# Performance work log

Measured on AMD Instinct MI355X. Metric: run time of the kernel, lower is better.

## Reference

```python
import jax, jax.numpy as jnp
import numpy as np

WD, WH, WW = 2, 7, 7          # window size (D, H, W)
SD, SH, SW = 1, 3, 3          # shift size
DIM, NH = 128, 4              # channels, heads
B, D, H, W = 8, 8, 56, 56     # input dims
N = WD * WH * WW              # tokens per window = 98
HIDDEN = int(DIM * 4.0)


def _rel_index_np():
    coords = np.stack(np.meshgrid(np.arange(WD), np.arange(WH), np.arange(WW), indexing='ij'))
    coords = coords.reshape(3, -1)                      # [3, N]
    rel = (coords[:, :, None] - coords[:, None, :]).transpose(1, 2, 0)  # [N, N, 3]
    rel[:, :, 0] += WD - 1
    rel[:, :, 1] += WH - 1
    rel[:, :, 2] += WW - 1
    rel[:, :, 0] *= (2 * WH - 1) * (2 * WW - 1)
    rel[:, :, 1] *= (2 * WW - 1)
    return rel.sum(-1).astype(np.int32)                 # [N, N]


def _window_partition_np(x):
    b, d, h, w, c = x.shape
    x = x.reshape(b, d // WD, WD, h // WH, WH, w // WW, WW, c)
    return x.transpose(0, 1, 3, 5, 2, 4, 6, 7).reshape(-1, N, c)


def _attn_mask_np():
    img = np.zeros((1, D, H, W, 1), np.float32)
    cnt = 0
    for ds in (slice(0, -WD), slice(-WD, -SD), slice(-SD, None)):
        for hs in (slice(0, -WH), slice(-WH, -SH), slice(-SH, None)):
            for ws in (slice(0, -WW), slice(-WW, -SW), slice(-SW, None)):
                img[:, ds, hs, ws, :] = cnt
                cnt += 1
    mw = _window_partition_np(img).reshape(-1, N)       # [nW, N]
    am = mw[:, None, :] - mw[:, :, None]
    return np.where(am != 0, -100.0, 0.0).astype(np.float32)  # [nW, N, N]


def setup_inputs() -> dict:
    key = jax.random.key(0)
    ks = jax.random.split(key, 8)
    s = 0.02
    return {
        'x': jax.random.normal(ks[0], (B, D, H, W, DIM), jnp.float32),
        'mask_matrix': jnp.asarray(_attn_mask_np()),
        'rel_index': jnp.asarray(_rel_index_np()),
        'norm1_g': jnp.ones((DIM,), jnp.float32),
        'norm1_b': jnp.zeros((DIM,), jnp.float32),
        'qkv_w': s * jax.random.normal(ks[1], (DIM, 3 * DIM), jnp.float32),
        'qkv_b': jnp.zeros((3 * DIM,), jnp.float32),
        'rpb': s * jax.random.normal(ks[2], ((2 * WD - 1) * (2 * WH - 1) * (2 * WW - 1), NH), jnp.float32),
        'proj_w': s * jax.random.normal(ks[3], (DIM, DIM), jnp.float32),
        'proj_b': jnp.zeros((DIM,), jnp.float32),
        'norm2_g': jnp.ones((DIM,), jnp.float32),
        'norm2_b': jnp.zeros((DIM,), jnp.float32),
        'fc1_w': s * jax.random.normal(ks[4], (DIM, HIDDEN), jnp.float32),
        'fc1_b': jnp.zeros((HIDDEN,), jnp.float32),
        'fc2_w': s * jax.random.normal(ks[5], (HIDDEN, DIM), jnp.float32),
        'fc2_b': jnp.zeros((DIM,), jnp.float32),
    }


def _ln(x, g, b):
    mu = jnp.mean(x, -1, keepdims=True)
    v = jnp.mean((x - mu) ** 2, -1, keepdims=True)
    return (x - mu) * jax.lax.rsqrt(v + 1e-5) * g + b


def _partition(x):
    b, d, h, w, c = x.shape
    x = x.reshape(b, d // WD, WD, h // WH, WH, w // WW, WW, c)
    return x.transpose(0, 1, 3, 5, 2, 4, 6, 7).reshape(-1, N, c)


def _reverse(win, b, d, h, w):
    c = win.shape[-1]
    x = win.reshape(b, d // WD, h // WH, w // WW, WD, WH, WW, c)
    return x.transpose(0, 1, 4, 2, 5, 3, 6, 7).reshape(b, d, h, w, c)


def _forward(x, mask_matrix, rel_index, norm1_g, norm1_b, qkv_w, qkv_b, rpb,
             proj_w, proj_b, norm2_g, norm2_b, fc1_w, fc1_b, fc2_w, fc2_b):
    b, d, h, w, c = x.shape
    shortcut = x
    y = _ln(x, norm1_g, norm1_b)
    # pad to multiples of window size (static; 0 for chosen dims)
    pd, ph, pw = (-d) % WD, (-h) % WH, (-w) % WW
    y = jnp.pad(y, ((0, 0), (0, pd), (0, ph), (0, pw), (0, 0)))
    dp, hp, wp = d + pd, h + ph, w + pw
    # cyclic shift
    y = jnp.roll(y, (-SD, -SH, -SW), axis=(1, 2, 3))
    win = _partition(y)                                   # [Bw, N, C]
    bw = win.shape[0]
    hd = c // NH
    qkv = (win @ qkv_w + qkv_b).reshape(bw, N, 3, NH, hd).transpose(2, 0, 3, 1, 4)
    q, k, v = qkv[0] * (hd ** -0.5), qkv[1], qkv[2]       # [Bw, NH, N, hd]
    attn = jnp.einsum('bhnd,bhmd->bhnm', q, k)            # [Bw, NH, N, N]
    bias = rpb[rel_index].transpose(2, 0, 1)              # [NH, N, N]
    attn = attn + bias[None]
    nw = mask_matrix.shape[0]
    attn = attn.reshape(bw // nw, nw, NH, N, N) + mask_matrix[None, :, None]
    attn = jax.nn.softmax(attn.reshape(bw, NH, N, N), axis=-1)
    o = jnp.einsum('bhnm,bhmd->bhnd', attn, v).transpose(0, 2, 1, 3).reshape(bw, N, c)
    o = o @ proj_w + proj_b
    y = _reverse(o, b, dp, hp, wp)
    y = jnp.roll(y, (SD, SH, SW), axis=(1, 2, 3))[:, :d, :h, :w, :]
    x1 = shortcut + y                                     # first residual
    z = _ln(x1, norm2_g, norm2_b)
    z = jax.nn.gelu(z @ fc1_w + fc1_b, approximate=False)
    # NOTE: source code's call() returns drop_path(mlp(norm2(x))) WITHOUT the
    # second residual add; we replicate exactly (drop_path is Identity at rate 0).
    return z @ fc2_w + fc2_b


def reference(x, mask_matrix, rel_index, norm1_g, norm1_b, qkv_w, qkv_b, rpb,
              proj_w, proj_b, norm2_g, norm2_b, fc1_w, fc1_b, fc2_w, fc2_b):
    return _forward(x, mask_matrix, rel_index, norm1_g, norm1_b, qkv_w, qkv_b,
                    rpb, proj_w, proj_b, norm2_g, norm2_b, fc1_w, fc1_b, fc2_w, fc2_b)


if __name__ == '__main__':
    out = reference(**setup_inputs())
    print(out.shape)
```

## Files before the change

### kernel.cpp

```cpp
#include <hip/hip_runtime.h>
#include <hip/hip_bf16.h>

typedef __attribute__((ext_vector_type(8))) short bf16x8;
typedef __attribute__((ext_vector_type(4))) float f32x4;

#define MFMA(a,b,c) __builtin_amdgcn_mfma_f32_16x16x32_bf16((a),(b),(c),0,0,0)
#define WAVE_LDS_FENCE() do { asm volatile("s_waitcnt lgkmcnt(0)" ::: "memory"); \
                              __builtin_amdgcn_sched_barrier(0); } while (0)

static constexpr int NTOK = 8 * 8 * 56 * 56;
static constexpr int NT   = 98;
static constexpr int NWIN = 2048;
static constexpr int NN   = NT * NT;

__device__ __forceinline__ unsigned short f2bf(float f) {
  unsigned r;
  asm("v_cvt_pk_bf16_f32 %0, %1, %1" : "=v"(r) : "v"(f));
  return (unsigned short)r;
}
__device__ __forceinline__ unsigned f2bf2(float lo, float hi) {
  unsigned r;
  asm("v_cvt_pk_bf16_f32 %0, %1, %2" : "=v"(r) : "v"(lo), "v"(hi));
  return r;
}
__device__ __forceinline__ float bf2f(unsigned short s) {
  union { unsigned u; float f; } v; v.u = ((unsigned)s) << 16; return v.f;
}
union U8 { unsigned u[4]; bf16x8 v; };

__global__ __launch_bounds__(256) void k0_prep(
    const float* __restrict__ qkv_w, const float* __restrict__ proj_w,
    const float* __restrict__ fc1_w, const float* __restrict__ fc2_w,
    const float* __restrict__ n1g, const float* __restrict__ n1b,
    const float* __restrict__ qkv_b,
    unsigned short* __restrict__ qkvT, unsigned short* __restrict__ projT,
    unsigned short* __restrict__ fc1T, unsigned short* __restrict__ fc2T,
    float* __restrict__ qbb) {
  int idx = blockIdx.x * 256 + threadIdx.x;
  if (idx < 384 * 128) { int n = idx >> 7, k = idx & 127; qkvT[idx] = f2bf(qkv_w[k * 384 + n] * n1g[k]); }
  if (idx < 128 * 128) { int n = idx >> 7, k = idx & 127; projT[idx] = f2bf(proj_w[k * 128 + n]); }
  if (idx < 512 * 128) { int n = idx >> 7, k = idx & 127; fc1T[idx] = f2bf(fc1_w[k * 512 + n]); }
  if (idx < 128 * 512) { int n = idx >> 9, k = idx & 511; fc2T[idx] = f2bf(fc2_w[k * 128 + n]); }
  if (idx < 384) {
    float acc = qkv_b[idx];
    for (int k = 0; k < 128; ++k) acc += n1b[k] * qkv_w[k * 384 + idx];
    qbb[idx] = acc;
  }
}

__global__ __launch_bounds__(256) void k0b_cmb(
    const int* __restrict__ rel, const float* __restrict__ rpb,
    const float* __restrict__ mask, unsigned short* __restrict__ cmb) {
  int idx = blockIdx.x * 256 + threadIdx.x;
  if (idx >= 4 * 256 * NN) return;
  int h = idx / (256 * NN);
  int rem = idx - h * 256 * NN;
  int wb = rem / NN, r = rem - wb * NN;
  cmb[idx] = f2bf(rpb[rel[r] * 4 + h] + mask[(size_t)wb * NN + r]);
}

__global__ __launch_bounds__(256, 2) void k2_qkv(
    const float* __restrict__ x, const unsigned short* __restrict__ qkvT,
    const float* __restrict__ qbb,
    unsigned short* __restrict__ q, unsigned short* __restrict__ k,
    unsigned short* __restrict__ v) {
  __shared__ __align__(16) unsigned short wsW[64 * 136];
  int tid = threadIdx.x, wv = tid >> 6, lane = tid & 63;
  int l15 = lane & 15, lhi = lane >> 4;
  int mbase = blockIdx.x * 128 + wv * 32;

  bf16x8 afr[2][4];
#pragma unroll
  for (int mt = 0; mt < 2; ++mt) {
    int row = mbase + mt * 16 + l15;
    int widx = row / NT, n = row - widx * NT;
    int bb = widx >> 8, wb = widx & 255;
    int dW = wb >> 6, hW = (wb >> 3) & 7, wW = wb & 7;
    int dr = n / 49, rem = n - dr * 49, hr = rem / 7, wr = rem - hr * 7;
    int dsh = (dW * 2 + dr + 1) & 7;
    int hs = hW * 7 + hr + 3; if (hs >= 56) hs -= 56;
    int wsv = wW * 7 + wr + 3; if (wsv >= 56) wsv -= 56;
    size_t srow = ((size_t)(bb * 8 + dsh) * 56 + hs) * 56 + wsv;
    const float* xr = x + srow * 128 + lhi * 8;
    float xv[4][8];
    float s = 0.f, ss = 0.f;
#pragma unroll
    for (int ks = 0; ks < 4; ++ks) {
      float4 lo = *(const float4*)(xr + ks * 32);
      float4 hi = *(const float4*)(xr + ks * 32 + 4);
      xv[ks][0] = lo.x; xv[ks][1] = lo.y; xv[ks][2] = lo.z; xv[ks][3] = lo.w;
      xv[ks][4] = hi.x; xv[ks][5] = hi.y; xv[ks][6] = hi.z; xv[ks][7] = hi.w;
#pragma unroll
      for (int e = 0; e < 8; ++e) { s += xv[ks][e]; ss += xv[ks][e] * xv[ks][e]; }
    }
    s += __shfl_xor(s, 16);  ss += __shfl_xor(ss, 16);
    s += __shfl_xor(s, 32);  ss += __shfl_xor(ss, 32);
    float mu = s * (1.f / 128.f);
    float var = ss * (1.f / 128.f) - mu * mu;
    float inv = __builtin_amdgcn_rsqf(var + 1e-5f);
#pragma unroll
    for (int ks = 0; ks < 4; ++ks) {
      U8 t;
#pragma unroll
      for (int p = 0; p < 4; ++p)
        t.u[p] = f2bf2((xv[ks][2 * p] - mu) * inv, (xv[ks][2 * p + 1] - mu) * inv);
      afr[mt][ks] = t.v;
    }
  }

  int rbase[2][4];
#pragma unroll
  for (int mt = 0; mt < 2; ++mt)
#pragma unroll
    for (int j = 0; j < 4; ++j) {
      int r = mbase + mt * 16 + lhi * 4 + j;
      int widx = r / NT, n = r - widx * NT;
      rbase[mt][j] = widx * 392 + n;
    }

  bf16x8 pf[4];
#pragma unroll
  for (int u = 0; u < 4; ++u) pf[u] = *(const bf16x8*)(qkvT + u * 2048 + tid * 8);

  for (int ch = 0; ch < 6; ++ch) {
#pragma unroll
    for (int u = 0; u < 4; ++u) {
      int flat = u * 2048 + tid * 8;
      *(bf16x8*)(&wsW[(flat >> 7) * 136 + (flat & 127)]) = pf[u];
    }
    __syncthreads();
    if (ch < 5) {
#pragma unroll
      for (int u = 0; u < 4; ++u)
        pf[u] = *(const bf16x8*)(qkvT + (ch + 1) * 8192 + u * 2048 + tid * 8);
    }
    f32x4 acc[2][4] = {};
#pragma unroll
    for (int ks = 0; ks < 4; ++ks)
#pragma unroll
      for (int nt = 0; nt < 4; ++nt) {
        bf16x8 bfr = *(const bf16x8*)(&wsW[(nt * 16 + l15) * 136 + ks * 32 + lhi * 8]);
#pragma unroll
        for (int mt = 0; mt < 2; ++mt)
          acc[mt][nt] = MFMA(afr[mt][ks], bfr, acc[mt][nt]);
      }
#pragma unroll
    for (int nt = 0; nt < 4; ++nt) {
      int col = ch * 64 + nt * 16 + l15;
      int which = col >> 7, head = (col >> 5) & 3, hd = col & 31;
      unsigned short* outb = which == 0 ? q : (which == 1 ? k : v);
      float scale = which == 0 ? 0.17677669529663687f : 1.0f;
      float bias = qbb[col];
#pragma unroll
      for (int mt = 0; mt < 2; ++mt)
#pragma unroll
        for (int j = 0; j < 4; ++j) {
          float val = (acc[mt][nt][j] + bias) * scale;
          outb[(size_t)(rbase[mt][j] + head * 98) * 32 + hd] = f2bf(val);
        }
    }
    __syncthreads();
  }
}

__global__ __launch_bounds__(512) void k3_attn(
    const unsigned short* __restrict__ q, const unsigned short* __restrict__ kk,
    const unsigned short* __restrict__ vv, const unsigned short* __restrict__ cmb,
    unsigned short* __restrict__ out) {
  __shared__ __align__(16) unsigned short Vt[32 * 140];
  __shared__ __align__(16) unsigned short Pw[7][16 * 140];
  int bid = blockIdx.x;
  int widx = bid >> 2, head = bid & 3;
  int wb = widx & 255;
  size_t base = (size_t)(widx * 4 + head) * NT * 32;
  int tid = threadIdx.x, wv = tid >> 6, lane = tid & 63;
  int l15 = lane & 15, lhi = lane >> 4;

  for (int idx = tid; idx < NT * 32; idx += 512) {
    int j = idx >> 5, d = idx & 31;
    Vt[d * 140 + j] = vv[base + idx];
  }
  for (int idx = tid; idx < 32 * 30; idx += 512) {
    int d = idx / 30, j = 98 + idx % 30;
    Vt[d * 140 + j] = 0;
  }
  __syncthreads();
  if (wv >= 7) return;

  const unsigned short* cw = cmb + ((size_t)(head << 8) + wb) * NN;
  unsigned short* P = Pw[wv];
  int mb = wv * 16;

  bf16x8 afr = *(const bf16x8*)(q + base + (size_t)(mb + l15) * 32 + lhi * 8);
  f32x4 sfr[7];
#pragma unroll
  for (int nt = 0; nt < 7; ++nt) {
    bf16x8 bfr = *(const bf16x8*)(kk + base + (size_t)(nt * 16 + l15) * 32 + lhi * 8);
    f32x4 zz = {};
    sfr[nt] = MFMA(afr, bfr, zz);
  }
#pragma unroll
  for (int j = 0; j < 4; ++j) {
    int i = mb + lhi * 4 + j;
    int ic = i < 97 ? i : 97;
    float sv[7];
#pragma unroll
    for (int nt = 0; nt < 7; ++nt) {
      int colc = nt * 16 + l15;
      int jc = colc < 97 ? colc : 97;
      float s = fminf(fmaxf(sfr[nt][j], -1e4f), 1e4f);
      float bm = bf2f(cw[ic * NT + jc]);
      sv[nt] = (i < NT && colc < NT) ? (s + bm) : -1e30f;
    }
    float mx = sv[0];
#pragma unroll
    for (int nt = 1; nt < 7; ++nt) mx = fmaxf(mx, sv[nt]);
#pragma unroll
    for (int m2 = 1; m2 < 16; m2 <<= 1) mx = fmaxf(mx, __shfl_xor(mx, m2));
    float sum = 0.f, p[7];
#pragma unroll
    for (int nt = 0; nt < 7; ++nt) { p[nt] = __expf(sv[nt] - mx); sum += p[nt]; }
#pragma unroll
    for (int m2 = 1; m2 < 16; m2 <<= 1) sum += __shfl_xor(sum, m2);
    float inv = __builtin_amdgcn_rcpf(sum);
    int iloc = lhi * 4 + j;
#pragma unroll
    for (int nt = 0; nt < 7; ++nt)
      P[iloc * 140 + nt * 16 + l15] = f2bf(p[nt] * inv);
    P[iloc * 140 + 112 + l15] = 0;
  }
  WAVE_LDS_FENCE();

  f32x4 ofr[2] = {};
#pragma unroll
  for (int ks = 0; ks < 4; ++ks) {
    bf16x8 pafr = *(const bf16x8*)(P + l15 * 140 + ks * 32 + lhi * 8);
#pragma unroll
    for (int nt = 0; nt < 2; ++nt) {
      bf16x8 bfr = *(const bf16x8*)(Vt + (nt * 16 + l15) * 140 + ks * 32 + lhi * 8);
      ofr[nt] = MFMA(pafr, bfr, ofr[nt]);
    }
  }
#pragma unroll
  for (int nt = 0; nt < 2; ++nt)
#pragma unroll
    for (int j = 0; j < 4; ++j) {
      int n = mb + lhi * 4 + j;
      if (n < NT) {
        int d = nt * 16 + l15;
        out[(size_t)(widx * NT + n) * 128 + head * 32 + d] = f2bf(ofr[nt][j]);
      }
    }
}

__global__ __launch_bounds__(256, 3) void k4_proj_ln(
    const unsigned short* __restrict__ ao, const unsigned short* __restrict__ projT,
    const float* __restrict__ proj_b, const float* __restrict__ x,
    const float* __restrict__ g2, const float* __restrict__ b2,
    unsigned short* __restrict__ z) {
  __shared__ __align__(16) unsigned short wsW[128 * 136];
  int tid = threadIdx.x, wv = tid >> 6, lane = tid & 63;
  int l15 = lane & 15, lhi = lane >> 4;
  int mbase = blockIdx.x * 128 + wv * 32;

#pragma unroll
  for (int u = 0; u < 8; ++u) {
    int flat = u * 2048 + tid * 8;
    *(bf16x8*)(&wsW[(flat >> 7) * 136 + (flat & 127)]) = *(const bf16x8*)(projT + flat);
  }
  bf16x8 afr[2][4];
#pragma unroll
  for (int mt = 0; mt < 2; ++mt)
#pragma unroll
    for (int ks = 0; ks < 4; ++ks)
      afr[mt][ks] = *(const bf16x8*)(ao + (size_t)(mbase + mt * 16 + l15) * 128 + ks * 32 + lhi * 8);
  __syncthreads();

  f32x4 acc[2][8] = {};
#pragma unroll
  for (int ks = 0; ks < 4; ++ks)
#pragma unroll
    for (int nt = 0; nt < 8; ++nt) {
      bf16x8 bfr = *(const bf16x8*)(&wsW[(nt * 16 + l15) * 136 + ks * 32 + lhi * 8]);
#pragma unroll
      for (int mt = 0; mt < 2; ++mt)
        acc[mt][nt] = MFMA(afr[mt][ks], bfr, acc[mt][nt]);
    }

#pragma unroll
  for (int mt = 0; mt < 2; ++mt)
#pragma unroll
    for (int j = 0; j < 4; ++j) {
      int t = mbase + mt * 16 + lhi * 4 + j;
      int widx = t / NT, n = t - widx * NT;
      int bb = widx >> 8, wb = widx & 255;
      int dW = wb >> 6, hW = (wb >> 3) & 7, wW = wb & 7;
      int dr = n / 49, rem = n - dr * 49, hr = rem / 7, wr = rem - hr * 7;
      int d = (dW * 2 + dr + 1) & 7;
      int h = hW * 7 + hr + 3; if (h >= 56) h -= 56;
      int w = wW * 7 + wr + 3; if (w >= 56) w -= 56;
      size_t srow = ((size_t)(bb * 8 + d) * 56 + h) * 56 + w;
      float vals[8], s = 0.f, ss = 0.f;
#pragma unroll
      for (int nt = 0; nt < 8; ++nt) {
        int colc = nt * 16 + l15;
        float val = acc[mt][nt][j] + proj_b[colc] + x[srow * 128 + colc];
        vals[nt] = val; s += val; ss += val * val;
      }
#pragma unroll
      for (int m2 = 1; m2 < 16; m2 <<= 1) { s += __shfl_xor(s, m2); ss += __shfl_xor(ss, m2); }
      float mu = s * (1.f / 128.f);
      float var = ss * (1.f / 128.f) - mu * mu;
      float inv = __builtin_amdgcn_rsqf(var + 1e-5f);
#pragma unroll
      for (int nt = 0; nt < 8; ++nt) {
        int colc = nt * 16 + l15;
        z[srow * 128 + colc] = f2bf((vals[nt] - mu) * inv * g2[colc] + b2[colc]);
      }
    }
}

__global__ __launch_bounds__(256, 2) void k5_mlp(
    const unsigned short* __restrict__ z, const unsigned short* __restrict__ fc1T,
    const float* __restrict__ fc1_b, const unsigned short* __restrict__ fc2T,
    const float* __restrict__ fc2_b, float* __restrict__ out) {
  __shared__ __align__(16) unsigned short wsA[64 * 132];
  __shared__ __align__(16) unsigned short wsB[128 * 68];
  __shared__ __align__(16) unsigned short hl[4][32 * 70];
  int tid = threadIdx.x, wv = tid >> 6, lane = tid & 63;
  int l15 = lane & 15, lhi = lane >> 4;
  int mbase = blockIdx.x * 128 + wv * 32;
  unsigned short* hw = hl[wv];

  bf16x8 afr[2][4];
#pragma unroll
  for (int mt = 0; mt < 2; ++mt)
#pragma unroll
    for (int ks = 0; ks < 4; ++ks)
      afr[mt][ks] = *(const bf16x8*)(z + (size_t)(mbase + mt * 16 + l15) * 128 + ks * 32 + lhi * 8);

  bf16x8 pfA[4], pfB[4];
#pragma unroll
  for (int u = 0; u < 4; ++u) pfA[u] = *(const bf16x8*)(fc1T + u * 2048 + tid * 8);
#pragma unroll
  for (int u = 0; u < 4; ++u) {
    int flat = u * 2048 + tid * 8;
    pfB[u] = *(const bf16x8*)(fc2T + (size_t)(flat >> 6) * 512 + (flat & 63));
  }

  f32x4 oacc[2][8] = {};
  for (int ch = 0; ch < 8; ++ch) {
#pragma unroll
    for (int u = 0; u < 4; ++u) {
      int flat = u * 2048 + tid * 8;
      *(bf16x8*)(&wsA[(flat >> 7) * 132 + (flat & 127)]) = pfA[u];
      *(bf16x8*)(&wsB[(flat >> 6) * 68 + (flat & 63)]) = pfB[u];
    }
    __syncthreads();
    if (ch < 7) {
#pragma unroll
      for (int u = 0; u < 4; ++u)
        pfA[u] = *(const bf16x8*)(fc1T + (ch + 1) * 8192 + u * 2048 + tid * 8);
#pragma unroll
      for (int u = 0; u < 4; ++u) {
        int flat = u * 2048 + tid * 8;
        pfB[u] = *(const bf16x8*)(fc2T + (size_t)(flat >> 6) * 512 + (ch + 1) * 64 + (flat & 63));
      }
    }
    f32x4 hacc[2][4] = {};
#pragma unroll
    for (int ks = 0; ks < 4; ++ks)
#pragma unroll
      for (int nt = 0; nt < 4; ++nt) {
        bf16x8 bfr = *(const bf16x8*)(&wsA[(nt * 16 + l15) * 132 + ks * 32 + lhi * 8]);
#pragma unroll
        for (int mt = 0; mt < 2; ++mt)
          hacc[mt][nt] = MFMA(afr[mt][ks], bfr, hacc[mt][nt]);
      }
#pragma unroll
    for (int mt = 0; mt < 2; ++mt)
#pragma unroll
      for (int nt = 0; nt < 4; ++nt)
#pragma unroll
        for (int j = 0; j < 4; ++j) {
          int r = mt * 16 + lhi * 4 + j;
          int hcol = ch * 64 + nt * 16 + l15;
          float hv = hacc[mt][nt][j] + fc1_b[hcol];
          float targ = hv * (1.5957691216f + 0.0713548162f * hv * hv);
          float gv = hv * __builtin_amdgcn_rcpf(1.0f + __expf(-targ));
          hw[r * 70 + nt * 16 + l15] = f2bf(gv);
        }
    WAVE_LDS_FENCE();
#pragma unroll
    for (int ks = 0; ks < 2; ++ks) {
      bf16x8 a2[2];
#pragma unroll
      for (int mt = 0; mt < 2; ++mt)
        a2[mt] = *(const bf16x8*)(&hw[(mt * 16 + l15) * 70 + ks * 32 + lhi * 8]);
#pragma unroll
      for (int nt = 0; nt < 8; ++nt) {
        bf16x8 bfr = *(const bf16x8*)(&wsB[(nt * 16 + l15) * 68 + ks * 32 + lhi * 8]);
#pragma unroll
        for (int mt = 0; mt < 2; ++mt)
          oacc[mt][nt] = MFMA(a2[mt], bfr, oacc[mt][nt]);
      }
    }
    WAVE_LDS_FENCE();
    __syncthreads();
  }
#pragma unroll
  for (int mt = 0; mt < 2; ++mt)
#pragma unroll
    for (int nt = 0; nt < 8; ++nt)
#pragma unroll
      for (int j = 0; j < 4; ++j) {
        int r = mbase + mt * 16 + lhi * 4 + j;
        out[(size_t)r * 128 + nt * 16 + l15] = oacc[mt][nt][j] + fc2_b[nt * 16 + l15];
      }
}

extern "C" void kernel_launch(void* const* d_in, const int* in_sizes, int n_in,
                              void* d_out, int out_size, void* d_ws, size_t ws_size,
                              hipStream_t stream) {
  const float* x      = (const float*)d_in[0];
  const float* mask   = (const float*)d_in[1];
  const int*   rel    = (const int*)d_in[2];
  const float* n1g    = (const float*)d_in[3];
  const float* n1b    = (const float*)d_in[4];
  const float* qkv_w  = (const float*)d_in[5];
  const float* qkv_b  = (const float*)d_in[6];
  const float* rpb    = (const float*)d_in[7];
  const float* proj_w = (const float*)d_in[8];
  const float* proj_b = (const float*)d_in[9];
  const float* n2g    = (const float*)d_in[10];
  const float* n2b    = (const float*)d_in[11];
  const float* fc1_w  = (const float*)d_in[12];
  const float* fc1_b  = (const float*)d_in[13];
  const float* fc2_w  = (const float*)d_in[14];
  const float* fc2_b  = (const float*)d_in[15];
  float* out = (float*)d_out;

  char* ws = (char*)d_ws;
  const size_t SZ = (size_t)NTOK * 128 * 2;
  unsigned short* win   = (unsigned short*)(ws);
  unsigned short* qb    = (unsigned short*)(ws + SZ);
  unsigned short* kb    = (unsigned short*)(ws + 2 * SZ);
  unsigned short* vb    = (unsigned short*)(ws + 3 * SZ);
  unsigned short* qkvT  = (unsigned short*)(ws + 4 * SZ);
  unsigned short* projT = qkvT + 384 * 128;
  unsigned short* fc1T  = projT + 128 * 128;
  unsigned short* fc2T  = fc1T + 512 * 128;
  unsigned short* cmb   = fc2T + 128 * 512;
  float* qbb            = (float*)(cmb + (size_t)4 * 256 * NN);
  unsigned short* ao = win;
  unsigned short* zb = qb;

  k0_prep<<<256, 256, 0, stream>>>(qkv_w, proj_w, fc1_w, fc2_w, n1g, n1b, qkv_b,
                                   qkvT, projT, fc1T, fc2T, qbb);
  k0b_cmb<<<(4 * 256 * NN + 255) / 256, 256, 0, stream>>>(rel, rpb, mask, cmb);
  k2_qkv<<<NTOK / 128, 256, 0, stream>>>(x, qkvT, qbb, qb, kb, vb);
  k3_attn<<<NWIN * 4, 512, 0, stream>>>(qb, kb, vb, cmb, ao);
  k4_proj_ln<<<NTOK / 128, 256, 0, stream>>>(ao, projT, proj_b, x, n2g, n2b, zb);
  k5_mlp<<<NTOK / 128, 256, 0, stream>>>(zb, fc1T, fc1_b, fc2T, fc2_b, out);
}
```

Measured before the change: 436.8 us.

## Stage proj+LN epilogue through LDS for coalesced I/O; widen MLP blocks to 512 threads

The proj+LN2 epilogue now writes accumulators (plus bias) to a per-wave LDS bounce buffer. Each group of four lanes then reads a full 128-channel row, so the residual read of x and the bf16 write of z become wide vectorized accesses instead of scattered 4-byte ones. The MLP kernel doubles its block to 512 threads (8 waves), which halves the per-block fc1/fc2 weight staging traffic per row processed. The cost is extra LDS traffic and fences, and the larger MLP block may lower occupancy given its register and LDS use.

Measured after the change: 409.2 us. 1.07x faster.

```diff
diff --git a/kernel.cpp b/kernel.cpp
--- a/kernel.cpp
+++ b/kernel.cpp
@@ -27,6 +27,17 @@
   union { unsigned u; float f; } v; v.u = ((unsigned)s) << 16; return v.f;
 }
 union U8 { unsigned u[4]; bf16x8 v; };
+
+__device__ __forceinline__ size_t srow_of(int t) {
+  int widx = t / NT, n = t - widx * NT;
+  int bb = widx >> 8, wb = widx & 255;
+  int dW = wb >> 6, hW = (wb >> 3) & 7, wW = wb & 7;
+  int dr = n / 49, rem = n - dr * 49, hr = rem / 7, wr = rem - hr * 7;
+  int dsh = (dW * 2 + dr + 1) & 7;
+  int hs = hW * 7 + hr + 3; if (hs >= 56) hs -= 56;
+  int wsv = wW * 7 + wr + 3; if (wsv >= 56) wsv -= 56;
+  return ((size_t)(bb * 8 + dsh) * 56 + hs) * 56 + wsv;
+}
 
 __global__ __launch_bounds__(256) void k0_prep(
     const float* __restrict__ qkv_w, const float* __restrict__ proj_w,
@@ -73,14 +84,7 @@
 #pragma unroll
   for (int mt = 0; mt < 2; ++mt) {
     int row = mbase + mt * 16 + l15;
-    int widx = row / NT, n = row - widx * NT;
-    int bb = widx >> 8, wb = widx & 255;
-    int dW = wb >> 6, hW = (wb >> 3) & 7, wW = wb & 7;
-    int dr = n / 49, rem = n - dr * 49, hr = rem / 7, wr = rem - hr * 7;
-    int dsh = (dW * 2 + dr + 1) & 7;
-    int hs = hW * 7 + hr + 3; if (hs >= 56) hs -= 56;
-    int wsv = wW * 7 + wr + 3; if (wsv >= 56) wsv -= 56;
-    size_t srow = ((size_t)(bb * 8 + dsh) * 56 + hs) * 56 + wsv;
+    size_t srow = srow_of(row);
     const float* xr = x + srow * 128 + lhi * 8;
     float xv[4][8];
     float s = 0.f, ss = 0.f;
@@ -286,50 +290,70 @@
       for (int mt = 0; mt < 2; ++mt)
         acc[mt][nt] = MFMA(afr[mt][ks], bfr, acc[mt][nt]);
     }
-
-#pragma unroll
-  for (int mt = 0; mt < 2; ++mt)
-#pragma unroll
-    for (int j = 0; j < 4; ++j) {
-      int t = mbase + mt * 16 + lhi * 4 + j;
-      int widx = t / NT, n = t - widx * NT;
-      int bb = widx >> 8, wb = widx & 255;
-      int dW = wb >> 6, hW = (wb >> 3) & 7, wW = wb & 7;
-      int dr = n / 49, rem = n - dr * 49, hr = rem / 7, wr = rem - hr * 7;
-      int d = (dW * 2 + dr + 1) & 7;
-      int h = hW * 7 + hr + 3; if (h >= 56) h -= 56;
-      int w = wW * 7 + wr + 3; if (w >= 56) w -= 56;
-      size_t srow = ((size_t)(bb * 8 + d) * 56 + h) * 56 + w;
-      float vals[8], s = 0.f, ss = 0.f;
-#pragma unroll
-      for (int nt = 0; nt < 8; ++nt) {
-        int colc = nt * 16 + l15;
-        float val = acc[mt][nt][j] + proj_b[colc] + x[srow * 128 + colc];
-        vals[nt] = val; s += val; ss += val * val;
-      }
-#pragma unroll
-      for (int m2 = 1; m2 < 16; m2 <<= 1) { s += __shfl_xor(s, m2); ss += __shfl_xor(ss, m2); }
-      float mu = s * (1.f / 128.f);
-      float var = ss * (1.f / 128.f) - mu * mu;
-      float inv = __builtin_amdgcn_rsqf(var + 1e-5f);
-#pragma unroll
-      for (int nt = 0; nt < 8; ++nt) {
-        int colc = nt * 16 + l15;
-        z[srow * 128 + colc] = f2bf((vals[nt] - mu) * inv * g2[colc] + b2[colc]);
-      }
-    }
-}
-
-__global__ __launch_bounds__(256, 2) void k5_mlp(
+  __syncthreads();
+
+  float* bounce = (float*)wsW + wv * (16 * 132);
+  float pb[8];
+#pragma unroll
+  for (int nt = 0; nt < 8; ++nt) pb[nt] = proj_b[nt * 16 + l15];
+
+  int rl = lane >> 2, c0 = (lane & 3) * 32;
+#pragma unroll
+  for (int mt = 0; mt < 2; ++mt) {
+#pragma unroll
+    for (int nt = 0; nt < 8; ++nt)
+#pragma unroll
+      for (int j = 0; j < 4; ++j)
+        bounce[(lhi * 4 + j) * 132 + nt * 16 + l15] = acc[mt][nt][j] + pb[nt];
+    WAVE_LDS_FENCE();
+
+    int t = mbase + mt * 16 + rl;
+    size_t srow = srow_of(t);
+    const float* xr = x + srow * 128 + c0;
+    float vals[32];
+    float s = 0.f, ss = 0.f;
+#pragma unroll
+    for (int i = 0; i < 8; ++i) {
+      float4 pv = *(const float4*)(bounce + rl * 132 + c0 + 4 * i);
+      float4 xv = *(const float4*)(xr + 4 * i);
+      float a0 = pv.x + xv.x, a1 = pv.y + xv.y, a2 = pv.z + xv.z, a3 = pv.w + xv.w;
+      vals[4 * i] = a0; vals[4 * i + 1] = a1; vals[4 * i + 2] = a2; vals[4 * i + 3] = a3;
+      s += a0 + a1 + a2 + a3;
+      ss += a0 * a0 + a1 * a1 + a2 * a2 + a3 * a3;
+    }
+    s += __shfl_xor(s, 1);  ss += __shfl_xor(ss, 1);
+    s += __shfl_xor(s, 2);  ss += __shfl_xor(ss, 2);
+    float mu = s * (1.f / 128.f);
+    float var = ss * (1.f / 128.f) - mu * mu;
+    float inv = __builtin_amdgcn_rsqf(var + 1e-5f);
+    unsigned pk[16];
+#pragma unroll
+    for (int i = 0; i < 8; ++i) {
+      float4 g = *(const float4*)(g2 + c0 + 4 * i);
+      float4 b = *(const float4*)(b2 + c0 + 4 * i);
+      pk[2 * i]     = f2bf2((vals[4 * i]     - mu) * inv * g.x + b.x,
+                            (vals[4 * i + 1] - mu) * inv * g.y + b.y);
+      pk[2 * i + 1] = f2bf2((vals[4 * i + 2] - mu) * inv * g.z + b.z,
+                            (vals[4 * i + 3] - mu) * inv * g.w + b.w);
+    }
+    unsigned* zp = (unsigned*)(z + srow * 128 + c0);
+#pragma unroll
+    for (int i = 0; i < 4; ++i)
+      *(uint4*)(zp + 4 * i) = make_uint4(pk[4 * i], pk[4 * i + 1], pk[4 * i + 2], pk[4 * i + 3]);
+    WAVE_LDS_FENCE();
+  }
+}
+
+__global__ __launch_bounds__(512, 2) void k5_mlp(
     const unsigned short* __restrict__ z, const unsigned short* __restrict__ fc1T,
     const float* __restrict__ fc1_b, const unsigned short* __restrict__ fc2T,
     const float* __restrict__ fc2_b, float* __restrict__ out) {
   __shared__ __align__(16) unsigned short wsA[64 * 132];
   __shared__ __align__(16) unsigned short wsB[128 * 68];
-  __shared__ __align__(16) unsigned short hl[4][32 * 70];
+  __shared__ __align__(16) unsigned short hl[8][32 * 70];
   int tid = threadIdx.x, wv = tid >> 6, lane = tid & 63;
   int l15 = lane & 15, lhi = lane >> 4;
-  int mbase = blockIdx.x * 128 + wv * 32;
+  int mbase = blockIdx.x * 256 + wv * 32;
   unsigned short* hw = hl[wv];
 
   bf16x8 afr[2][4];
@@ -339,31 +363,31 @@
     for (int ks = 0; ks < 4; ++ks)
       afr[mt][ks] = *(const bf16x8*)(z + (size_t)(mbase + mt * 16 + l15) * 128 + ks * 32 + lhi * 8);
 
-  bf16x8 pfA[4], pfB[4];
-#pragma unroll
-  for (int u = 0; u < 4; ++u) pfA[u] = *(const bf16x8*)(fc1T + u * 2048 + tid * 8);
-#pragma unroll
-  for (int u = 0; u < 4; ++u) {
-    int flat = u * 2048 + tid * 8;
+  bf16x8 pfA[2], pfB[2];
+#pragma unroll
+  for (int u = 0; u < 2; ++u) pfA[u] = *(const bf16x8*)(fc1T + u * 4096 + tid * 8);
+#pragma unroll
+  for (int u = 0; u < 2; ++u) {
+    int flat = u * 4096 + tid * 8;
     pfB[u] = *(const bf16x8*)(fc2T + (size_t)(flat >> 6) * 512 + (flat & 63));
   }
 
   f32x4 oacc[2][8] = {};
   for (int ch = 0; ch < 8; ++ch) {
 #pragma unroll
-    for (int u = 0; u < 4; ++u) {
-      int flat = u * 2048 + tid * 8;
+    for (int u = 0; u < 2; ++u) {
+      int flat = u * 4096 + tid * 8;
       *(bf16x8*)(&wsA[(flat >> 7) * 132 + (flat & 127)]) = pfA[u];
       *(bf16x8*)(&wsB[(flat >> 6) * 68 + (flat & 63)]) = pfB[u];
     }
     __syncthreads();
     if (ch < 7) {
 #pragma unroll
-      for (int u = 0; u < 4; ++u)
-        pfA[u] = *(const bf16x8*)(fc1T + (ch + 1) * 8192 + u * 2048 + tid * 8);
-#pragma unroll
-      for (int u = 0; u < 4; ++u) {
-        int flat = u * 2048 + tid * 8;
+      for (int u = 0; u < 2; ++u)
+        pfA[u] = *(const bf16x8*)(fc1T + (ch + 1) * 8192 + u * 4096 + tid * 8);
+#pragma unroll
+      for (int u = 0; u < 2; ++u) {
+        int flat = u * 4096 + tid * 8;
         pfB[u] = *(const bf16x8*)(fc2T + (size_t)(flat >> 6) * 512 + (ch + 1) * 64 + (flat & 63));
       }
     }
@@ -461,5 +485,5 @@
   k2_qkv<<<NTOK / 128, 256, 0, stream>>>(x, qkvT, qbb, qb, kb, vb);
   k3_attn<<<NWIN * 4, 512, 0, stream>>>(qb, kb, vb, cmb, ao);
   k4_proj_ln<<<NTOK / 128, 256, 0, stream>>>(ao, projT, proj_b, x, n2g, n2b, zb);
-  k5_mlp<<<NTOK / 128, 256, 0, stream>>>(zb, fc1T, fc1_b, fc2T, fc2_b, out);
-}
+  k5_mlp<<<NTOK / 256, 512, 0, stream>>>(zb, fc1T, fc1_b, fc2T, fc2_b, out);
+}
```
